# Kernel optimization log

Measured on AMD Instinct MI355X. Metric: run time of the kernel, lower is better.

## Reference

```python
import jax, jax.numpy as jnp
import numpy as np

T, B, D, H = 512, 64, 768, 768


def setup_inputs() -> dict:
    key = jax.random.key(0)
    ks = jax.random.split(key, 9)
    s = 1.0 / np.sqrt(D + H)  # ~torch Linear init scale
    inp = {"x": jax.random.normal(ks[0], (T, B, D), dtype=jnp.float32)}
    names = ["Wf", "bf", "Wi", "bi", "Wg", "bg", "Wo", "bo"]
    for j, n in enumerate(names):
        shape = (H, D + H) if n.startswith("W") else (H,)
        inp[n] = jax.random.uniform(ks[j + 1], shape, jnp.float32, -s, s)
    return inp


def reference(x, Wf, bf, Wi, bi, Wg, bg, Wo, bo):
    # x: [T, B, D] time-major. Classical LSTM cell with 4 separate gate linears.
    Bsz = x.shape[1]
    h0 = jnp.zeros((Bsz, H), x.dtype)
    c0 = jnp.zeros((Bsz, H), x.dtype)

    def step(carry, xt):
        h, c = carry
        comb = jnp.concatenate([xt, h], axis=1)  # [B, D+H]
        f = jax.nn.sigmoid(comb @ Wf.T + bf)
        i = jax.nn.sigmoid(comb @ Wi.T + bi)
        g = jnp.tanh(comb @ Wg.T + bg)
        o = jax.nn.sigmoid(comb @ Wo.T + bo)
        c = f * c + i * g
        h = o * jnp.tanh(c)
        return (h, c), h

    (hT, cT), outputs = jax.lax.scan(step, (h0, c0), x)
    return outputs, (hT, cT)
```

## Files before the change

### kernel.cpp

```cpp
#include <hip/hip_runtime.h>
#include <stdint.h>

typedef __attribute__((ext_vector_type(8))) short short8;
typedef __attribute__((ext_vector_type(4))) float f32x4;
typedef __attribute__((ext_vector_type(4))) unsigned short u16x4;

#define NWG 96

#define OFF_XBF   0UL
#define SZ_XBF    (512UL*64*768*2)
#define OFF_WXB   (OFF_XBF + SZ_XBF)
#define SZ_WB     (3072UL*768*2)
#define OFF_WHB   (OFF_WXB + SZ_WB)
#define OFF_BALL  (OFF_WHB + SZ_WB)
#define SZ_BALL   (3072UL*4)
#define OFF_XG    (OFF_BALL + SZ_BALL)
#define SZ_XG     (512UL*3072*64*2)
#define OFF_HBUF  (OFF_XG + SZ_XG)
#define SZ_HBUF   (2UL*64*768*2)
#define OFF_FLAGS (OFF_HBUF + SZ_HBUF)
#define SZ_FLAGS  (NWG*16UL*4)

__device__ __forceinline__ float bf2f(unsigned short u){
  union{unsigned int i; float f;} v; v.i = ((unsigned int)u)<<16; return v.f;
}
__device__ __forceinline__ unsigned short f2bf(float f){
  union{float f; unsigned int i;} v; v.f = f;
  unsigned int x = v.i;
  return (unsigned short)((x + 0x7fffu + ((x>>16)&1u)) >> 16);
}
__device__ __forceinline__ float sigm(float x){ return 1.0f/(1.0f + __expf(-x)); }
__device__ __forceinline__ float tanh_s(float x){
  float e = __expf(2.0f*fabsf(x));
  float r = 1.0f - 2.0f/(e+1.0f);
  return copysignf(r, x);
}
__device__ __forceinline__ f32x4 mfma16(short8 a, short8 b, f32x4 c){
  return __builtin_amdgcn_mfma_f32_16x16x32_bf16(a, b, c, 0, 0, 0);
}
__device__ __forceinline__ short8 ld_b128_sc(const unsigned short* p){
  short8 r;
  asm volatile("global_load_dwordx4 %0, %1, off sc0 sc1"
               : "=&v"(r) : "v"(p) : "memory");
  return r;
}
__device__ __forceinline__ void st_b128_sc(unsigned short* p, short8 v){
  asm volatile("global_store_dwordx4 %0, %1, off sc0 sc1"
               :: "v"(p), "v"(v) : "memory");
}

__global__ void k_conv_x(const float* __restrict__ x, unsigned short* __restrict__ xb, int n4){
  int i = blockIdx.x*blockDim.x + threadIdx.x;
  if (i >= n4) return;
  float4 v = ((const float4*)x)[i];
  u16x4 o = { f2bf(v.x), f2bf(v.y), f2bf(v.z), f2bf(v.w) };
  *(u16x4*)(xb + (size_t)i*4) = o;
}

__global__ void k_conv_w(const float* __restrict__ Wf, const float* __restrict__ Wi,
                         const float* __restrict__ Wg, const float* __restrict__ Wo,
                         unsigned short* __restrict__ Wxb, unsigned short* __restrict__ Whb){
  int i = blockIdx.x*blockDim.x + threadIdx.x;
  if (i >= 3072*192) return;
  int gj = i / 192; int kc = (i % 192)*4;
  int g = gj / 768, j = gj % 768;
  const float* W = (g==0)?Wf:(g==1)?Wi:(g==2)?Wg:Wo;
  float4 vx = *(const float4*)(W + (size_t)j*1536 + kc);
  float4 vh = *(const float4*)(W + (size_t)j*1536 + 768 + kc);
  u16x4 ox = {f2bf(vx.x),f2bf(vx.y),f2bf(vx.z),f2bf(vx.w)};
  u16x4 oh = {f2bf(vh.x),f2bf(vh.y),f2bf(vh.z),f2bf(vh.w)};
  *(u16x4*)(Wxb + (size_t)gj*768 + kc) = ox;
  *(u16x4*)(Whb + (size_t)gj*768 + kc) = oh;
}

__global__ void k_conv_b(const float* __restrict__ b0, const float* __restrict__ b1,
                         const float* __restrict__ b2, const float* __restrict__ b3,
                         float* __restrict__ ball){
  int i = blockIdx.x*blockDim.x + threadIdx.x;
  if (i >= 3072) return;
  int g = i/768, j = i%768;
  const float* b = (g==0)?b0:(g==1)?b1:(g==2)?b2:b3;
  ball[i] = b[j];
}

__global__ __launch_bounds__(256) void k_gemm_x(const unsigned short* __restrict__ xb,
        const unsigned short* __restrict__ Wxb, unsigned short* __restrict__ Xg){
  __shared__ __align__(16) short Ald[128*32];
  __shared__ __align__(16) short Bld[128*32];
  int blk = blockIdx.x;
  int bm = blk / 24, bn = blk % 24;
  size_t Mbase = (size_t)bm*128; int Nbase = bn*128;
  int tid = threadIdx.x; int w = tid>>6, l = tid&63;
  int wm = w&1, wn = w>>1, lr = l&15, lg = l>>4;
  f32x4 acc[4][4];
  #pragma unroll
  for (int a=0;a<4;++a)
    #pragma unroll
    for(int b2=0;b2<4;++b2) acc[a][b2] = (f32x4){0.f,0.f,0.f,0.f};
  int c0i = tid, c1i = tid+256;
  int r0 = c0i>>2, o0 = (c0i&3)*8;
  int r1 = c1i>>2, o1 = (c1i&3)*8;
  for (int kt=0; kt<24; ++kt) {
    int k0 = kt*32;
    short8 a0 = *(const short8*)(xb + (Mbase + r0)*768 + k0 + o0);
    short8 a1 = *(const short8*)(xb + (Mbase + r1)*768 + k0 + o1);
    short8 b0 = *(const short8*)(Wxb + (size_t)(Nbase + r0)*768 + k0 + o0);
    short8 b1 = *(const short8*)(Wxb + (size_t)(Nbase + r1)*768 + k0 + o1);
    __syncthreads();
    *(short8*)(Ald + r0*32 + o0) = a0;
    *(short8*)(Ald + r1*32 + o1) = a1;
    *(short8*)(Bld + r0*32 + o0) = b0;
    *(short8*)(Bld + r1*32 + o1) = b1;
    __syncthreads();
    short8 af[4], bfr[4];
    #pragma unroll
    for (int mi=0;mi<4;++mi) af[mi] = *(const short8*)(Ald + (wm*64+mi*16+lr)*32 + lg*8);
    #pragma unroll
    for (int ni=0;ni<4;++ni) bfr[ni] = *(const short8*)(Bld + (wn*64+ni*16+lr)*32 + lg*8);
    #pragma unroll
    for (int mi=0;mi<4;++mi)
      #pragma unroll
      for (int ni=0;ni<4;++ni)
        acc[mi][ni] = mfma16(af[mi], bfr[ni], acc[mi][ni]);
  }
  #pragma unroll
  for (int mi=0;mi<4;++mi){
    int m0 = (int)Mbase + wm*64 + mi*16 + lg*4;
    int t = m0>>6, b = m0&63;
    #pragma unroll
    for (int ni=0;ni<4;++ni){
      int col = Nbase + wn*64 + ni*16 + lr;
      u16x4 u = { f2bf(acc[mi][ni][0]), f2bf(acc[mi][ni][1]),
                  f2bf(acc[mi][ni][2]), f2bf(acc[mi][ni][3]) };
      *(u16x4*)(Xg + ((size_t)t*3072 + col)*64 + b) = u;
    }
  }
}

__global__ __launch_bounds__(512, 1) void k_lstm(const unsigned short* __restrict__ Xg,
     const unsigned short* __restrict__ Whb, const float* __restrict__ ball,
     unsigned short* __restrict__ hbuf, float* __restrict__ out, int* __restrict__ flags){
  __shared__ __align__(16) short Wl[32*776];
  __shared__ __align__(16) unsigned short hl[64*8];
  int s = blockIdx.x, tid = threadIdx.x;
  int w8 = tid>>6, l = tid&63;
  int m = w8 & 3, nh = w8 >> 2;
  int n0 = l & 15, lg = l >> 4;
  int gate = n0 >> 2;
  int jj4 = nh*4 + (n0 & 3);
  int j = s*8 + jj4;
  size_t gj = (size_t)gate*768 + j;
  int rB = jj4*4 + gate;

  for (int c = tid; c < 3072; c += 512){
    int r = c/96, off = (c%96)*8;
    int gt = r & 3, jq = r >> 2;
    short8 v = *(const short8*)(Whb + ((size_t)(gt*768 + s*8 + jq))*768 + off);
    *(short8*)(Wl + r*776 + off) = v;
  }
  __syncthreads();

  float bias = ball[gj];
  float cst[4] = {0.f, 0.f, 0.f, 0.f};
  int arow = m*16 + n0;
  int b4 = m*16 + lg*4;
  bool actv = (n0 < 4);
  u16x4 xg = *(const u16x4*)(Xg + gj*64 + b4);

  for (int t=0; t<512; ++t){
    const unsigned short* hb = hbuf + (size_t)(t&1)*(64*768);
    unsigned short* hn = hbuf + (size_t)((t+1)&1)*(64*768);
    short8 afr[24];
    #pragma unroll
    for (int kk=0; kk<24; ++kk)
      afr[kk] = ld_b128_sc(hb + arow*768 + kk*32 + lg*8);
    asm volatile("s_waitcnt vmcnt(0)" ::: "memory");
    __builtin_amdgcn_sched_barrier(0);
    f32x4 acc0 = {0.f,0.f,0.f,0.f}, acc1 = {0.f,0.f,0.f,0.f};
    #pragma unroll
    for (int kk=0; kk<24; kk+=2){
      short8 b0 = *(const short8*)(Wl + rB*776 + kk*32 + lg*8);
      short8 b1 = *(const short8*)(Wl + rB*776 + (kk+1)*32 + lg*8);
      acc0 = mfma16(afr[kk],   b0, acc0);
      acc1 = mfma16(afr[kk+1], b1, acc1);
    }
    f32x4 acc = acc0 + acc1;
    float av[4];
    #pragma unroll
    for (int r=0; r<4; ++r){
      float pre = acc[r] + bf2f(xg[r]) + bias;
      av[r] = (gate == 2) ? tanh_s(pre) : sigm(pre);
    }
    float hvv[4];
    #pragma unroll
    for (int r=0; r<4; ++r){
      float iv = __shfl_xor(av[r], 4);
      float gv = __shfl_xor(av[r], 8);
      float ov = __shfl_xor(av[r], 12);
      float cn = av[r]*cst[r] + iv*gv;
      float hv = ov * tanh_s(cn);
      if (actv){
        cst[r] = cn;
        hvv[r] = hv;
        if (t < 511) hl[(b4 + r)*8 + jj4] = f2bf(hv);
      }
    }
    if (t < 511){
      __syncthreads();
      if (w8 == 7){
        short8 hp = *(const short8*)(hl + l*8);
        st_b128_sc(hn + (size_t)l*768 + s*8, hp);
        asm volatile("s_waitcnt vmcnt(0)" ::: "memory");
        if (l == 0)
          __hip_atomic_store(&flags[s*16], t+1, __ATOMIC_RELAXED, __HIP_MEMORY_SCOPE_AGENT);
      }
      if (actv){
        #pragma unroll
        for (int r=0; r<4; ++r)
          out[((size_t)t*64 + b4 + r)*768 + j] = hvv[r];
      }
      u16x4 xgn = *(const u16x4*)(Xg + ((size_t)(t+1)*3072 + gj)*64 + b4);
      if (w8 == 0){
        int tgt = t+1;
        for (int it=0; it<(1<<14); ++it){
          int f1 = __hip_atomic_load(&flags[l*16], __ATOMIC_RELAXED, __HIP_MEMORY_SCOPE_AGENT);
          int f2 = (l<32) ? __hip_atomic_load(&flags[(64+l)*16], __ATOMIC_RELAXED, __HIP_MEMORY_SCOPE_AGENT) : tgt;
          if (__all(f1>=tgt && f2>=tgt)) break;
          __builtin_amdgcn_s_sleep(1);
        }
      }
      __syncthreads();
      xg = xgn;
    } else if (actv){
      #pragma unroll
      for (int r=0; r<4; ++r){
        int b = b4 + r;
        out[((size_t)t*64 + b)*768 + j] = hvv[r];
        out[(512UL*64 + b)*768 + j] = hvv[r];
        out[(512UL*64 + 64 + b)*768 + j] = cst[r];
      }
    }
  }
}

extern "C" void kernel_launch(void* const* d_in, const int* in_sizes, int n_in,
                              void* d_out, int out_size, void* d_ws, size_t ws_size,
                              hipStream_t stream){
  const float* x   = (const float*)d_in[0];
  const float* Wf  = (const float*)d_in[1];
  const float* bf_ = (const float*)d_in[2];
  const float* Wi  = (const float*)d_in[3];
  const float* bi_ = (const float*)d_in[4];
  const float* Wg  = (const float*)d_in[5];
  const float* bg_ = (const float*)d_in[6];
  const float* Wo  = (const float*)d_in[7];
  const float* bo_ = (const float*)d_in[8];
  char* ws = (char*)d_ws;
  if (ws_size < OFF_FLAGS + SZ_FLAGS) return;
  unsigned short* xb   = (unsigned short*)(ws + OFF_XBF);
  unsigned short* Wxb  = (unsigned short*)(ws + OFF_WXB);
  unsigned short* Whb  = (unsigned short*)(ws + OFF_WHB);
  float*          ball = (float*)(ws + OFF_BALL);
  unsigned short* Xg   = (unsigned short*)(ws + OFF_XG);
  unsigned short* hbuf = (unsigned short*)(ws + OFF_HBUF);
  int*            flags= (int*)(ws + OFF_FLAGS);
  float* out = (float*)d_out;

  (void)hipMemsetAsync(hbuf, 0, SZ_HBUF + SZ_FLAGS, stream);
  k_conv_x<<<24576, 256, 0, stream>>>(x, xb, 6291456);
  k_conv_w<<<2304, 256, 0, stream>>>(Wf, Wi, Wg, Wo, Wxb, Whb);
  k_conv_b<<<12, 256, 0, stream>>>(bf_, bi_, bg_, bo_, ball);
  k_gemm_x<<<6144, 256, 0, stream>>>(xb, Wxb, Xg);
  k_lstm<<<NWG, 512, 0, stream>>>(Xg, Whb, ball, hbuf, out, flags);
}
```

Before: 4.823 ms.

## Use per-timestep hidden-state buffers and flags to allow cached h loads

Each timestep now gets its own hidden-state slice and its own set of arrival flags. These live in workspace regions that are dead once the input GEMM has finished. Because addresses are never reused, the per-step h reads switch from cache-bypassing sc0/sc1 asm loads to plain vector loads. The explicit waitcnt and sched_barrier are dropped, so the compiler can overlap these loads with the MFMAs. The flag check becomes a nonzero test on a fresh array per step, at the cost of a larger memset and more memory footprint.

```diff
diff --git a/kernel.cpp b/kernel.cpp
--- a/kernel.cpp
+++ b/kernel.cpp
@@ -16,10 +16,10 @@
 #define SZ_BALL   (3072UL*4)
 #define OFF_XG    (OFF_BALL + SZ_BALL)
 #define SZ_XG     (512UL*3072*64*2)
-#define OFF_HBUF  (OFF_XG + SZ_XG)
-#define SZ_HBUF   (2UL*64*768*2)
-#define OFF_FLAGS (OFF_HBUF + SZ_HBUF)
-#define SZ_FLAGS  (NWG*16UL*4)
+#define OFF_END   (OFF_XG + SZ_XG)
+
+#define HSTRIDE   49152
+#define FSTRIDE   1536
 
 __device__ __forceinline__ float bf2f(unsigned short u){
   union{unsigned int i; float f;} v; v.i = ((unsigned int)u)<<16; return v.f;
@@ -37,12 +37,6 @@
 }
 __device__ __forceinline__ f32x4 mfma16(short8 a, short8 b, f32x4 c){
   return __builtin_amdgcn_mfma_f32_16x16x32_bf16(a, b, c, 0, 0, 0);
-}
-__device__ __forceinline__ short8 ld_b128_sc(const unsigned short* p){
-  short8 r;
-  asm volatile("global_load_dwordx4 %0, %1, off sc0 sc1"
-               : "=&v"(r) : "v"(p) : "memory");
-  return r;
 }
 __device__ __forceinline__ void st_b128_sc(unsigned short* p, short8 v){
   asm volatile("global_store_dwordx4 %0, %1, off sc0 sc1"
@@ -139,7 +133,7 @@
 
 __global__ __launch_bounds__(512, 1) void k_lstm(const unsigned short* __restrict__ Xg,
      const unsigned short* __restrict__ Whb, const float* __restrict__ ball,
-     unsigned short* __restrict__ hbuf, float* __restrict__ out, int* __restrict__ flags){
+     unsigned short* __restrict__ hbase, float* __restrict__ out, int* __restrict__ flags){
   __shared__ __align__(16) short Wl[32*776];
   __shared__ __align__(16) unsigned short hl[64*8];
   int s = blockIdx.x, tid = threadIdx.x;
@@ -168,14 +162,12 @@
   u16x4 xg = *(const u16x4*)(Xg + gj*64 + b4);
 
   for (int t=0; t<512; ++t){
-    const unsigned short* hb = hbuf + (size_t)(t&1)*(64*768);
-    unsigned short* hn = hbuf + (size_t)((t+1)&1)*(64*768);
+    const unsigned short* hb = hbase + (size_t)t*HSTRIDE;
+    unsigned short* hn = hbase + (size_t)(t+1)*HSTRIDE;
     short8 afr[24];
     #pragma unroll
     for (int kk=0; kk<24; ++kk)
-      afr[kk] = ld_b128_sc(hb + arow*768 + kk*32 + lg*8);
-    asm volatile("s_waitcnt vmcnt(0)" ::: "memory");
-    __builtin_amdgcn_sched_barrier(0);
+      afr[kk] = *(const short8*)(hb + arow*768 + kk*32 + lg*8);
     f32x4 acc0 = {0.f,0.f,0.f,0.f}, acc1 = {0.f,0.f,0.f,0.f};
     #pragma unroll
     for (int kk=0; kk<24; kk+=2){
@@ -212,7 +204,8 @@
         st_b128_sc(hn + (size_t)l*768 + s*8, hp);
         asm volatile("s_waitcnt vmcnt(0)" ::: "memory");
         if (l == 0)
-          __hip_atomic_store(&flags[s*16], t+1, __ATOMIC_RELAXED, __HIP_MEMORY_SCOPE_AGENT);
+          __hip_atomic_store(&flags[(size_t)t*FSTRIDE + s*16], 1,
+                             __ATOMIC_RELAXED, __HIP_MEMORY_SCOPE_AGENT);
       }
       if (actv){
         #pragma unroll
@@ -221,11 +214,11 @@
       }
       u16x4 xgn = *(const u16x4*)(Xg + ((size_t)(t+1)*3072 + gj)*64 + b4);
       if (w8 == 0){
-        int tgt = t+1;
+        const int* fl = flags + (size_t)t*FSTRIDE;
         for (int it=0; it<(1<<14); ++it){
-          int f1 = __hip_atomic_load(&flags[l*16], __ATOMIC_RELAXED, __HIP_MEMORY_SCOPE_AGENT);
-          int f2 = (l<32) ? __hip_atomic_load(&flags[(64+l)*16], __ATOMIC_RELAXED, __HIP_MEMORY_SCOPE_AGENT) : tgt;
-          if (__all(f1>=tgt && f2>=tgt)) break;
+          int f1 = __hip_atomic_load(&fl[l*16], __ATOMIC_RELAXED, __HIP_MEMORY_SCOPE_AGENT);
+          int f2 = (l<32) ? __hip_atomic_load(&fl[(64+l)*16], __ATOMIC_RELAXED, __HIP_MEMORY_SCOPE_AGENT) : 1;
+          if (__all(f1!=0 && f2!=0)) break;
           __builtin_amdgcn_s_sleep(1);
         }
       }
@@ -256,20 +249,21 @@
   const float* Wo  = (const float*)d_in[7];
   const float* bo_ = (const float*)d_in[8];
   char* ws = (char*)d_ws;
-  if (ws_size < OFF_FLAGS + SZ_FLAGS) return;
+  if (ws_size < OFF_END) return;
   unsigned short* xb   = (unsigned short*)(ws + OFF_XBF);
   unsigned short* Wxb  = (unsigned short*)(ws + OFF_WXB);
   unsigned short* Whb  = (unsigned short*)(ws + OFF_WHB);
   float*          ball = (float*)(ws + OFF_BALL);
   unsigned short* Xg   = (unsigned short*)(ws + OFF_XG);
-  unsigned short* hbuf = (unsigned short*)(ws + OFF_HBUF);
-  int*            flags= (int*)(ws + OFF_FLAGS);
   float* out = (float*)d_out;
 
-  (void)hipMemsetAsync(hbuf, 0, SZ_HBUF + SZ_FLAGS, stream);
   k_conv_x<<<24576, 256, 0, stream>>>(x, xb, 6291456);
   k_conv_w<<<2304, 256, 0, stream>>>(Wf, Wi, Wg, Wo, Wxb, Whb);
   k_conv_b<<<12, 256, 0, stream>>>(bf_, bi_, bg_, bo_, ball);
   k_gemm_x<<<6144, 256, 0, stream>>>(xb, Wxb, Xg);
-  k_lstm<<<NWG, 512, 0, stream>>>(Xg, Whb, ball, hbuf, out, flags);
-}
+  (void)hipMemsetAsync(ws + OFF_XBF, 0, 98304, stream);
+  (void)hipMemsetAsync(ws + OFF_WXB, 0, 512UL*FSTRIDE*4, stream);
+  k_lstm<<<NWG, 512, 0, stream>>>(Xg, Whb, ball,
+                                  (unsigned short*)(ws + OFF_XBF), out,
+                                  (int*)(ws + OFF_WXB));
+}
```

After: 4.544 ms. 1.06x faster.
